# Kernel optimization log

Measured on AMD Instinct MI355X. Metric: run time of the kernel, lower is better.

Reference implementation:

```python
import jax, jax.numpy as jnp
import numpy as np

E = 65536      # num edges
T = 262144     # num triplets
H = 128        # hidden_channels
D = 64         # int_emb_size
C = 8          # basis_emb_size
NR = 6         # num_radial
NS = 7         # num_spherical
NB = 6         # len(bt_list) = num_BT + 1
BT_LIST = (-1, 0, 1, 2, 3, 4)
NBS = 1        # num_before_skip (also used for after-skip list in original code)


def setup_inputs() -> dict:
    key = jax.random.key(0)
    ks = iter(jax.random.split(key, 40))
    s = 0.05
    p = lambda shape: jax.random.normal(next(ks), shape, dtype=jnp.float32) * s
    inp = dict(
        x=jax.random.normal(next(ks), (E, H), dtype=jnp.float32),
        rbf=jax.random.normal(next(ks), (E, NR), dtype=jnp.float32),
        sbf=jax.random.normal(next(ks), (T, NS * NR), dtype=jnp.float32),
        idx_kj=jax.random.randint(next(ks), (T,), 0, E),
        idx_ji=jax.random.randint(next(ks), (T,), 0, E),
        bt=jax.random.randint(next(ks), (E,), 0, 5),
        lambda_d=1,
        alpha=jnp.float32(0.7),
        # per-branch stacked weights (6 branches)
        W_kj=p((NB, H, H)), b_kj=jnp.zeros((NB, H), jnp.float32),
        W_rbf1=p((NB, NR, C)), W_rbf2=p((NB, C, H)),
        W_sbf1=p((NB, NS * NR, C)), W_sbf2=p((NB, C, D)),
        W_down=p((NB, H, D)),
        W_ji=p((H, H)), b_ji=jnp.zeros((H,), jnp.float32),
        W_up=p((D, H)),
        rb1_w=p((NBS, H, H)), rb1_b=jnp.zeros((NBS, H), jnp.float32),
        rb2_w=p((NBS, H, H)), rb2_b=jnp.zeros((NBS, H), jnp.float32),
        W_lin=p((H, H)), b_lin=jnp.zeros((H,), jnp.float32),
        ra1_w=p((NBS, H, H)), ra1_b=jnp.zeros((NBS, H), jnp.float32),
        ra2_w=p((NBS, H, H)), ra2_b=jnp.zeros((NBS, H), jnp.float32),
    )
    return inp


def reference(x, rbf, sbf, idx_kj, idx_ji, bt, lambda_d, alpha,
              W_kj, b_kj, W_rbf1, W_rbf2, W_sbf1, W_sbf2, W_down,
              W_ji, b_ji, W_up, rb1_w, rb1_b, rb2_w, rb2_b,
              W_lin, b_lin, ra1_w, ra1_b, ra2_w, ra2_b):
    act = jax.nn.silu

    x_ji = act(x @ W_ji + b_ji)                                  # [E,H]

    # per-branch edge transforms, vectorized over the 6 branches (axis b)
    tmp = act(jnp.einsum('eh,bhg->beg', x, W_kj) + b_kj[:, None, :])   # [B,E,H]
    rbf_p = jnp.einsum('er,brc->bec', rbf, W_rbf1)                     # [B,E,C]
    rbf_p = jnp.einsum('bec,bcg->beg', rbf_p, W_rbf2)                  # [B,E,H]
    tmp = tmp * rbf_p
    down = act(jnp.einsum('beh,bhd->bed', tmp, W_down))                # [B,E,D]

    sbf_p = jnp.einsum('ts,bsc->btc', sbf, W_sbf1)                     # [B,T,C]
    sbf_p = jnp.einsum('btc,bcd->btd', sbf_p, W_sbf2)                  # [B,T,D]

    spe = down[:, idx_kj, :] * sbf_p                                   # [B,T,D]

    # last branch scattered with weight alpha
    x_kj_tot = alpha * jax.ops.segment_sum(spe[-1], idx_ji, num_segments=E)

    # per band-type masked scatter with weight (1 - alpha)
    bt_trip = bt[idx_kj]                                               # [T]
    for b, btv in enumerate(BT_LIST):
        m = (bt_trip == btv).astype(x.dtype)[:, None]
        x_kj_tot = x_kj_tot + (1.0 - alpha) * jax.ops.segment_sum(
            spe[b] * m, idx_ji, num_segments=E)

    x_kj = act(x_kj_tot @ W_up)                                        # [E,H]
    h = x_ji + x_kj
    for i in range(rb1_w.shape[0]):
        h = h + act(act(h @ rb1_w[i] + rb1_b[i]) @ rb2_w[i] + rb2_b[i])
    h = act(h @ W_lin + b_lin) + x
    for i in range(ra1_w.shape[0]):
        h = h + act(act(h @ ra1_w[i] + ra1_b[i]) @ ra2_w[i] + ra2_b[i])
    return h
```

## Files before the change

kernel.cpp:

```cpp
#include <hip/hip_runtime.h>
#include <hip/hip_bf16.h>
#include <stdint.h>

typedef __bf16 bf16_t;
typedef bf16_t bf16x8 __attribute__((ext_vector_type(8)));
typedef bf16_t bf16x2 __attribute__((ext_vector_type(2)));
typedef float f32x4 __attribute__((ext_vector_type(4)));

#define E_N 65536
#define T_N 262144

__device__ __forceinline__ float silu_f(float v) {
  return v / (1.0f + __expf(-v));
}

__device__ __forceinline__ int permrow(int n) {
  return (n & ~31) | ((n & 1) << 4) | ((n & 30) >> 1);
}

__device__ __forceinline__ uint32_t pack_bf16(float a, float b) {
  union { bf16x2 h; uint32_t u; } u;
  u.h[0] = (bf16_t)a; u.h[1] = (bf16_t)b;
  return u.u;
}

template<int KI, int NTJ>
__device__ __forceinline__ void gemm_tile(const bf16_t* A, const bf16_t* B,
                                          int mb, int nb, int l16, int q,
                                          f32x4 (&acc)[2][NTJ]) {
#pragma unroll
  for (int kt = 0; kt < KI; ++kt) {
    const int sw = ((kt * 4 + q) ^ l16) << 3;
    bf16x8 a0 = *(const bf16x8*)(A + ((mb + l16) << 7) + sw);
    bf16x8 a1 = *(const bf16x8*)(A + ((mb + 16 + l16) << 7) + sw);
#pragma unroll
    for (int tj = 0; tj < NTJ; ++tj) {
      bf16x8 b = *(const bf16x8*)(B + ((nb + tj * 16 + l16) << 7) + sw);
      acc[0][tj] = __builtin_amdgcn_mfma_f32_16x16x32_bf16(a0, b, acc[0][tj], 0, 0, 0);
      acc[1][tj] = __builtin_amdgcn_mfma_f32_16x16x32_bf16(a1, b, acc[1][tj], 0, 0, 0);
    }
  }
}

template<int ROWS, int K8>
__device__ __forceinline__ void load_wT(bf16_t* dst, const bf16_t* src, int tid) {
  const uint4* s = (const uint4*)src;
#pragma unroll
  for (int i = tid; i < ROWS * K8; i += 256) {
    const int n = i / K8, k8 = i % K8;
    const int row = permrow(n);
    *(uint4*)(dst + (row << 7) + ((k8 ^ (row & 15)) << 3)) = s[i];
  }
}

template<int C4>
__device__ __forceinline__ void stage_x(bf16_t* dst, const float* src, int tid) {
  const float4* g = (const float4*)src;
#pragma unroll
  for (int i = tid; i < 64 * C4; i += 256) {
    const int row = i / C4, c4 = i % C4;
    float4 v = g[i];
    bf16_t t[4] = {(bf16_t)v.x, (bf16_t)v.y, (bf16_t)v.z, (bf16_t)v.w};
    *(uint2*)(dst + (row << 7) + ((((c4 >> 1) ^ (row & 15)) << 3) | ((c4 & 1) << 2))) =
        *(const uint2*)t;
  }
}

__global__ void prep_kernel(
    const float* __restrict__ W_ji, const float* __restrict__ W_kj,
    const float* __restrict__ W_down, const float* __restrict__ W_up,
    const float* __restrict__ rb1, const float* __restrict__ rb2,
    const float* __restrict__ W_lin, const float* __restrict__ ra1,
    const float* __restrict__ ra2, const float* __restrict__ W_rbf1,
    const float* __restrict__ W_rbf2,
    bf16_t* __restrict__ wjiT, bf16_t* __restrict__ wkjT,
    bf16_t* __restrict__ wdownT, bf16_t* __restrict__ wupT,
    bf16_t* __restrict__ rb1T, bf16_t* __restrict__ rb2T,
    bf16_t* __restrict__ linT, bf16_t* __restrict__ ra1T,
    bf16_t* __restrict__ ra2T, bf16_t* __restrict__ wcb)
{
  const int tid = threadIdx.x;
  if (blockIdx.x >= 112) {
    const int o = (blockIdx.x - 112) * 256 + tid;
    if (o < 640) {
      const int b = o >> 7, n = o & 127;
      bf16_t t[8];
#pragma unroll
      for (int r = 0; r < 6; ++r) {
        const float* w1 = W_rbf1 + (b + 1) * 48 + r * 8;
        const float* w2 = W_rbf2 + (b + 1) * 1024 + n;
        float s = 0.f;
#pragma unroll
        for (int c = 0; c < 8; ++c) s += w1[c] * w2[c * 128];
        t[r] = (bf16_t)s;
      }
      t[6] = (bf16_t)0.f; t[7] = (bf16_t)0.f;
      *(uint4*)(wcb + (b * 128 + n) * 8) = *(const uint4*)t;
    }
    return;
  }
  const int c = blockIdx.x * 256 + tid;
  const float* src; bf16_t* dst; int n, k8, N, K;
  if (c < 22528) {
    const int m = c >> 11, w = c & 2047;
    n = w >> 4; k8 = w & 15; N = 128; K = 128;
    if (m == 0)      { src = W_ji;  dst = wjiT; }
    else if (m <= 5) { src = W_kj + m * 16384; dst = wkjT + (m - 1) * 16384; }
    else if (m == 6) { src = rb1;   dst = rb1T; }
    else if (m == 7) { src = rb2;   dst = rb2T; }
    else if (m == 8) { src = W_lin; dst = linT; }
    else if (m == 9) { src = ra1;   dst = ra1T; }
    else             { src = ra2;   dst = ra2T; }
  } else if (c < 27648) {
    const int m = (c - 22528) >> 10, w = (c - 22528) & 1023;
    n = w >> 4; k8 = w & 15; N = 64; K = 128;
    src = W_down + (m + 1) * 8192; dst = wdownT + m * 8192;
  } else {
    const int w = c - 27648;
    n = w >> 3; k8 = w & 7; N = 128; K = 64;
    src = W_up; dst = wupT;
  }
  bf16_t t[8];
#pragma unroll
  for (int j = 0; j < 8; ++j) t[j] = (bf16_t)src[(k8 * 8 + j) * N + n];
  *(uint4*)(dst + n * K + k8 * 8) = *(const uint4*)t;
}

__global__ __launch_bounds__(256, 2)
void edge_kernel(const float* __restrict__ x, const float* __restrict__ rbf,
                 const float* __restrict__ b_kj, const float* __restrict__ b_ji,
                 const bf16_t* __restrict__ wjiT, const bf16_t* __restrict__ wkjT,
                 const bf16_t* __restrict__ wdownT, const bf16_t* __restrict__ wcb,
                 bf16_t* __restrict__ x_ji_out, bf16_t* __restrict__ down)
{
  __shared__ bf16_t xA[64 * 128];
  __shared__ bf16_t Wb[128 * 128];
  __shared__ bf16_t tmpA[64 * 128];
  __shared__ bf16_t rbfA[64 * 40];
  __shared__ bf16_t WcB[128 * 40];
  __shared__ float biasS[128];

  const int tid = threadIdx.x;
  const int lane = tid & 63, wv = tid >> 6;
  const int q = lane >> 4, l16 = lane & 15;
  const int mb = (wv >> 1) * 32, nb = (wv & 1) * 64;
  const int R = blockIdx.x * 64;
  const int br = blockIdx.y;

  stage_x<32>(xA, x + (size_t)R * 128, tid);
  if (br == 0) {
    load_wT<128, 16>(Wb, wjiT, tid);
    if (tid < 128) biasS[tid] = b_ji[tid];
  } else {
    load_wT<128, 16>(Wb, wkjT + (br - 1) * 16384, tid);
    if (tid < 128) biasS[tid] = b_kj[br * 128 + tid];
    const uint4 z = {0, 0, 0, 0};
    if (tid < 64) {
      const float* rg = rbf + (size_t)(R + tid) * 6;
      bf16_t t[8] = {(bf16_t)rg[0], (bf16_t)rg[1], (bf16_t)rg[2],
                     (bf16_t)rg[3], (bf16_t)rg[4], (bf16_t)rg[5],
                     (bf16_t)0.f, (bf16_t)0.f};
      *(uint4*)(rbfA + tid * 40)      = *(const uint4*)t;
      *(uint4*)(rbfA + tid * 40 + 8)  = z;
      *(uint4*)(rbfA + tid * 40 + 16) = z;
      *(uint4*)(rbfA + tid * 40 + 24) = z;
    } else if (tid >= 128) {
      const int n = tid - 128;
      const int row = permrow(n);
      uint4 w = ((const uint4*)(wcb + (size_t)(br - 1) * 1024))[n];
      *(uint4*)(WcB + row * 40)      = w;
      *(uint4*)(WcB + row * 40 + 8)  = z;
      *(uint4*)(WcB + row * 40 + 16) = z;
      *(uint4*)(WcB + row * 40 + 24) = z;
    }
  }
  __syncthreads();

  f32x4 acc[2][4] = {};
  gemm_tile<4, 4>(xA, Wb, mb, nb, l16, q, acc);

  if (br == 0) {
#pragma unroll
    for (int ti = 0; ti < 2; ++ti)
#pragma unroll
      for (int r = 0; r < 4; ++r) {
        const int row = mb + ti * 16 + q * 4 + r;
#pragma unroll
        for (int gl = 0; gl < 2; ++gl) {
          const int col0 = nb + gl * 32 + 2 * l16;
          const float2 b2 = *(const float2*)&biasS[col0];
          *(uint32_t*)&x_ji_out[(size_t)(R + row) * 128 + col0] =
              pack_bf16(silu_f(acc[ti][2 * gl][r] + b2.x),
                        silu_f(acc[ti][2 * gl + 1][r] + b2.y));
        }
      }
    return;
  }

  f32x4 accr[2][4] = {};
  {
    bf16x8 a0 = *(const bf16x8*)(rbfA + (mb + l16) * 40 + q * 8);
    bf16x8 a1 = *(const bf16x8*)(rbfA + (mb + 16 + l16) * 40 + q * 8);
#pragma unroll
    for (int tj = 0; tj < 4; ++tj) {
      bf16x8 b = *(const bf16x8*)(WcB + (nb + tj * 16 + l16) * 40 + q * 8);
      accr[0][tj] = __builtin_amdgcn_mfma_f32_16x16x32_bf16(a0, b, accr[0][tj], 0, 0, 0);
      accr[1][tj] = __builtin_amdgcn_mfma_f32_16x16x32_bf16(a1, b, accr[1][tj], 0, 0, 0);
    }
  }

#pragma unroll
  for (int ti = 0; ti < 2; ++ti)
#pragma unroll
    for (int r = 0; r < 4; ++r) {
      const int row = mb + ti * 16 + q * 4 + r;
#pragma unroll
      for (int gl = 0; gl < 2; ++gl) {
        const int col0 = nb + gl * 32 + 2 * l16;
        const float2 b2 = *(const float2*)&biasS[col0];
        const float v0 = silu_f(acc[ti][2 * gl][r] + b2.x) * accr[ti][2 * gl][r];
        const float v1 = silu_f(acc[ti][2 * gl + 1][r] + b2.y) * accr[ti][2 * gl + 1][r];
        *(uint32_t*)&tmpA[(row << 7) + ((((col0 >> 3) ^ (row & 15)) << 3) | (col0 & 7))] =
            pack_bf16(v0, v1);
      }
    }
  __syncthreads();
  load_wT<64, 16>(xA, wdownT + (br - 1) * 8192, tid);
  __syncthreads();

  const int nb2 = (wv & 1) * 32;
  f32x4 acc2[2][2] = {};
  gemm_tile<4, 2>(tmpA, xA, mb, nb2, l16, q, acc2);
#pragma unroll
  for (int ti = 0; ti < 2; ++ti)
#pragma unroll
    for (int r = 0; r < 4; ++r) {
      const int row = mb + ti * 16 + q * 4 + r;
      const int col0 = nb2 + 2 * l16;
      *(uint32_t*)&down[((size_t)(br - 1) * E_N + R + row) * 64 + col0] =
          pack_bf16(silu_f(acc2[ti][0][r]), silu_f(acc2[ti][1][r]));
    }
}

__global__ __launch_bounds__(256, 4)
void triplet_kernel(const float* __restrict__ sbf, const int* __restrict__ idx_kj,
                    const int* __restrict__ idx_ji, const int* __restrict__ bt,
                    const float* __restrict__ alpha_p,
                    const float* __restrict__ Wsbf1, const float* __restrict__ Wsbf2,
                    const bf16_t* __restrict__ down, float* __restrict__ xkj)
{
  __shared__ float s_sbf[64 * 44];
  __shared__ float s_W1[2016];
  __shared__ float s_W2[3072];
  __shared__ float s_c8[64 * 16];
  __shared__ int s_kj[64], s_ji[64], s_bs[64];

  const int tid = threadIdx.x;
  const int base = blockIdx.x * 64;

  for (int i = tid; i < 2016; i += 256) s_W1[i] = Wsbf1[i];
  for (int i = tid; i < 3072; i += 256) s_W2[i] = Wsbf2[i];
  if (tid < 64) {
    const int kj = idx_kj[base + tid];
    s_kj[tid] = kj;
    s_ji[tid] = idx_ji[base + tid];
    s_bs[tid] = bt[kj] + 1;
  }
  {
    const float2* sg = (const float2*)(sbf + (size_t)base * 42);
    for (int i = tid; i < 64 * 21; i += 256) {
      const int r = i / 21, c2 = i - r * 21;
      const float2 v = sg[i];
      s_sbf[r * 44 + c2 * 2] = v.x;
      s_sbf[r * 44 + c2 * 2 + 1] = v.y;
    }
  }
  __syncthreads();

  {
    const int i = tid >> 2;
    const int brr = (tid >> 1) & 1;
    const int cg = tid & 1;
    const int b = brr ? s_bs[i] : 5;
    const float* w = &s_W1[b * 336 + cg * 4];
    const float* sb = &s_sbf[i * 44];
    float a0 = 0.f, a1 = 0.f, a2 = 0.f, a3 = 0.f;
#pragma unroll
    for (int s = 0; s < 42; ++s) {
      const float sv = sb[s];
      const float* ws = w + s * 8;
      a0 += sv * ws[0]; a1 += sv * ws[1]; a2 += sv * ws[2]; a3 += sv * ws[3];
    }
    float* dc = &s_c8[i * 16 + brr * 8 + cg * 4];
    dc[0] = a0; dc[1] = a1; dc[2] = a2; dc[3] = a3;
  }
  __syncthreads();

  const float alpha = alpha_p[0];
  const float oma = 1.f - alpha;
  const int wv = tid >> 6, j = tid & 63;
  float w5[8];
#pragma unroll
  for (int c = 0; c < 8; ++c) w5[c] = s_W2[5 * 512 + c * 64 + j];

#pragma unroll 4
  for (int ii = 0; ii < 16; ++ii) {
    const int i = wv * 16 + ii;
    const int b = s_bs[i];
    const int kj = s_kj[i];
    const int ji = s_ji[i];
    const float* c8 = &s_c8[i * 16];
    float d5 = 0.f, db = 0.f;
#pragma unroll
    for (int c = 0; c < 8; ++c) {
      d5 += c8[c] * w5[c];
      db += c8[8 + c] * s_W2[b * 512 + c * 64 + j];
    }
    const float g5 = (float)down[((size_t)4 * E_N + kj) * 64 + j];
    const float gb = (float)down[((size_t)(b - 1) * E_N + kj) * 64 + j];
    const float r = alpha * g5 * d5 + oma * gb * db;
    unsafeAtomicAdd(&xkj[(size_t)ji * 64 + j], r);
  }
}

__global__ __launch_bounds__(256, 2)
void epi_kernel(const float* __restrict__ x, const bf16_t* __restrict__ x_ji,
                const float* __restrict__ xkj,
                const bf16_t* __restrict__ wupT,
                const bf16_t* __restrict__ rb1T, const float* __restrict__ rb1_b,
                const bf16_t* __restrict__ rb2T, const float* __restrict__ rb2_b,
                const bf16_t* __restrict__ linT, const float* __restrict__ lin_b,
                const bf16_t* __restrict__ ra1T, const float* __restrict__ ra1_b,
                const bf16_t* __restrict__ ra2T, const float* __restrict__ ra2_b,
                float* __restrict__ out)
{
  __shared__ bf16_t bufA[64 * 128];
  __shared__ bf16_t bufB[64 * 128];
  __shared__ bf16_t Wb[128 * 128];
  __shared__ float biasS[128];

  const int tid = threadIdx.x;
  const int lane = tid & 63, wv = tid >> 6;
  const int q = lane >> 4, l16 = lane & 15;
  const int mb = (wv >> 1) * 32, nb = (wv & 1) * 64;
  const int R = blockIdx.x * 64;

  stage_x<16>(bufA, xkj + (size_t)R * 64, tid);
  load_wT<128, 8>(Wb, wupT, tid);
  __syncthreads();

  f32x4 hreg[2][4];
  {
    f32x4 acc[2][4] = {};
    gemm_tile<2, 4>(bufA, Wb, mb, nb, l16, q, acc);
#pragma unroll
    for (int ti = 0; ti < 2; ++ti)
#pragma unroll
      for (int r = 0; r < 4; ++r) {
        const int row = mb + ti * 16 + q * 4 + r;
#pragma unroll
        for (int gl = 0; gl < 2; ++gl) {
          const int col0 = nb + gl * 32 + 2 * l16;
          union { uint32_t u; bf16x2 h; } xj;
          xj.u = *(const uint32_t*)&x_ji[(size_t)(R + row) * 128 + col0];
          const float h0 = (float)xj.h[0] + silu_f(acc[ti][2 * gl][r]);
          const float h1 = (float)xj.h[1] + silu_f(acc[ti][2 * gl + 1][r]);
          hreg[ti][2 * gl][r] = h0;
          hreg[ti][2 * gl + 1][r] = h1;
          *(uint32_t*)&bufB[(row << 7) + ((((col0 >> 3) ^ (row & 15)) << 3) | (col0 & 7))] =
              pack_bf16(h0, h1);
        }
      }
  }

#define EPI_STAGE(ASRC, WSRC, BIAS, BODY)                                        \
  __syncthreads();                                                               \
  load_wT<128, 16>(Wb, WSRC, tid);                                               \
  if (tid < 128) biasS[tid] = BIAS[tid];                                         \
  __syncthreads();                                                               \
  {                                                                              \
    f32x4 acc[2][4] = {};                                                        \
    gemm_tile<4, 4>(ASRC, Wb, mb, nb, l16, q, acc);                              \
    _Pragma("unroll")                                                            \
    for (int ti = 0; ti < 2; ++ti)                                               \
      _Pragma("unroll")                                                          \
      for (int r = 0; r < 4; ++r) {                                              \
        const int row = mb + ti * 16 + q * 4 + r;                                \
        _Pragma("unroll")                                                        \
        for (int gl = 0; gl < 2; ++gl) {                                         \
          const int col0 = nb + gl * 32 + 2 * l16;                               \
          const float2 b2 = *(const float2*)&biasS[col0];                        \
          const float g0 = acc[ti][2 * gl][r] + b2.x;                            \
          const float g1 = acc[ti][2 * gl + 1][r] + b2.y;                        \
          BODY                                                                   \
        }                                                                        \
      }                                                                          \
  }

  EPI_STAGE(bufB, rb1T, rb1_b, {
    *(uint32_t*)&bufA[(row << 7) + ((((col0 >> 3) ^ (row & 15)) << 3) | (col0 & 7))] =
        pack_bf16(silu_f(g0), silu_f(g1));
  })

  EPI_STAGE(bufA, rb2T, rb2_b, {
    const float h0 = hreg[ti][2 * gl][r] + silu_f(g0);
    const float h1 = hreg[ti][2 * gl + 1][r] + silu_f(g1);
    hreg[ti][2 * gl][r] = h0; hreg[ti][2 * gl + 1][r] = h1;
    *(uint32_t*)&bufB[(row << 7) + ((((col0 >> 3) ^ (row & 15)) << 3) | (col0 & 7))] =
        pack_bf16(h0, h1);
  })

  EPI_STAGE(bufB, linT, lin_b, {
    const float2 xv = *(const float2*)&x[(size_t)(R + row) * 128 + col0];
    const float h0 = silu_f(g0) + xv.x;
    const float h1 = silu_f(g1) + xv.y;
    hreg[ti][2 * gl][r] = h0; hreg[ti][2 * gl + 1][r] = h1;
    *(uint32_t*)&bufA[(row << 7) + ((((col0 >> 3) ^ (row & 15)) << 3) | (col0 & 7))] =
        pack_bf16(h0, h1);
  })

  EPI_STAGE(bufA, ra1T, ra1_b, {
    *(uint32_t*)&bufB[(row << 7) + ((((col0 >> 3) ^ (row & 15)) << 3) | (col0 & 7))] =
        pack_bf16(silu_f(g0), silu_f(g1));
  })

  EPI_STAGE(bufB, ra2T, ra2_b, {
    float2 o;
    o.x = hreg[ti][2 * gl][r] + silu_f(g0);
    o.y = hreg[ti][2 * gl + 1][r] + silu_f(g1);
    *(float2*)&out[(size_t)(R + row) * 128 + col0] = o;
  })
#undef EPI_STAGE
}

extern "C" void kernel_launch(void* const* d_in, const int* in_sizes, int n_in,
                              void* d_out, int out_size, void* d_ws, size_t ws_size,
                              hipStream_t stream)
{
  (void)in_sizes; (void)n_in; (void)out_size; (void)ws_size;
  const float* x      = (const float*)d_in[0];
  const float* rbf    = (const float*)d_in[1];
  const float* sbf    = (const float*)d_in[2];
  const int*   idx_kj = (const int*)d_in[3];
  const int*   idx_ji = (const int*)d_in[4];
  const int*   bt     = (const int*)d_in[5];
  const float* alpha  = (const float*)d_in[7];
  const float* W_kj   = (const float*)d_in[8];
  const float* b_kj   = (const float*)d_in[9];
  const float* W_rbf1 = (const float*)d_in[10];
  const float* W_rbf2 = (const float*)d_in[11];
  const float* W_sbf1 = (const float*)d_in[12];
  const float* W_sbf2 = (const float*)d_in[13];
  const float* W_down = (const float*)d_in[14];
  const float* W_ji   = (const float*)d_in[15];
  const float* b_ji   = (const float*)d_in[16];
  const float* W_up   = (const float*)d_in[17];
  const float* rb1_w  = (const float*)d_in[18];
  const float* rb1_b  = (const float*)d_in[19];
  const float* rb2_w  = (const float*)d_in[20];
  const float* rb2_b  = (const float*)d_in[21];
  const float* W_lin  = (const float*)d_in[22];
  const float* b_lin  = (const float*)d_in[23];
  const float* ra1_w  = (const float*)d_in[24];
  const float* ra1_b  = (const float*)d_in[25];
  const float* ra2_w  = (const float*)d_in[26];
  const float* ra2_b  = (const float*)d_in[27];

  char* ws = (char*)d_ws;
  bf16_t* down   = (bf16_t*)(ws);
  bf16_t* x_ji   = (bf16_t*)(ws + 41943040);
  float*  xkj    = (float*) (ws + 58720256);
  char* wbase    = ws + 75497472;
  bf16_t* wjiT   = (bf16_t*)(wbase + 0);
  bf16_t* wkjT   = (bf16_t*)(wbase + 32768);
  bf16_t* wdownT = (bf16_t*)(wbase + 196608);
  bf16_t* wupT   = (bf16_t*)(wbase + 278528);
  bf16_t* rb1T   = (bf16_t*)(wbase + 294912);
  bf16_t* rb2T   = (bf16_t*)(wbase + 327680);
  bf16_t* linT   = (bf16_t*)(wbase + 360448);
  bf16_t* ra1T   = (bf16_t*)(wbase + 393216);
  bf16_t* ra2T   = (bf16_t*)(wbase + 425984);
  bf16_t* wcb    = (bf16_t*)(wbase + 458752);

  hipMemsetAsync(xkj, 0, (size_t)E_N * 64 * 4, stream);
  prep_kernel<<<115, 256, 0, stream>>>(W_ji, W_kj, W_down, W_up, rb1_w, rb2_w,
                                       W_lin, ra1_w, ra2_w, W_rbf1, W_rbf2,
                                       wjiT, wkjT, wdownT, wupT, rb1T, rb2T,
                                       linT, ra1T, ra2T, wcb);
  edge_kernel<<<dim3(E_N / 64, 6), 256, 0, stream>>>(x, rbf, b_kj, b_ji, wjiT,
                                                     wkjT, wdownT, wcb, x_ji, down);
  triplet_kernel<<<T_N / 64, 256, 0, stream>>>(sbf, idx_kj, idx_ji, bt, alpha,
                                               W_sbf1, W_sbf2, down, xkj);
  epi_kernel<<<E_N / 64, 256, 0, stream>>>(x, x_ji, xkj, wupT, rb1T, rb1_b,
                                           rb2T, rb2_b, linT, b_lin,
                                           ra1T, ra1_b, ra2T, ra2_b,
                                           (float*)d_out);
}
```

Baseline: 377.6 us.

## Fold sbf weights into MFMA GEMM and read weights directly from global

The two sbf projections are premultiplied per branch in the prep kernel, so the triplet kernel now runs them as a bf16 MFMA GEMM over all five branch outputs instead of scalar FP32 loops through an 8-wide intermediate. The edge and epilogue kernels stop staging weight matrices in shared memory and load MFMA B-operands straight from global or L2 in a permuted layout. This removes the shared weight copies and their barriers, and cuts shared memory use so launch bounds can allow more resident blocks. In exchange, weights are re-read from cache by every wave, and the sbf product is rounded to bf16, which adds precision error.

```diff
diff --git a/kernel.cpp b/kernel.cpp
--- a/kernel.cpp
+++ b/kernel.cpp
@@ -24,10 +24,11 @@
   return u.u;
 }
 
-template<int KI, int NTJ>
-__device__ __forceinline__ void gemm_tile(const bf16_t* A, const bf16_t* B,
-                                          int mb, int nb, int l16, int q,
-                                          f32x4 (&acc)[2][NTJ]) {
+template<int KI, int NTJ, int BS>
+__device__ __forceinline__ void gemm_bg(const bf16_t* A, const bf16_t* __restrict__ Bg,
+                                        int mb, int nb, int l16, int q,
+                                        f32x4 (&acc)[2][NTJ]) {
+  const bf16_t* bp = Bg + (nb + l16) * BS + q * 8;
 #pragma unroll
   for (int kt = 0; kt < KI; ++kt) {
     const int sw = ((kt * 4 + q) ^ l16) << 3;
@@ -35,21 +36,10 @@
     bf16x8 a1 = *(const bf16x8*)(A + ((mb + 16 + l16) << 7) + sw);
 #pragma unroll
     for (int tj = 0; tj < NTJ; ++tj) {
-      bf16x8 b = *(const bf16x8*)(B + ((nb + tj * 16 + l16) << 7) + sw);
+      bf16x8 b = *(const bf16x8*)(bp + tj * 16 * BS + kt * 32);
       acc[0][tj] = __builtin_amdgcn_mfma_f32_16x16x32_bf16(a0, b, acc[0][tj], 0, 0, 0);
       acc[1][tj] = __builtin_amdgcn_mfma_f32_16x16x32_bf16(a1, b, acc[1][tj], 0, 0, 0);
     }
-  }
-}
-
-template<int ROWS, int K8>
-__device__ __forceinline__ void load_wT(bf16_t* dst, const bf16_t* src, int tid) {
-  const uint4* s = (const uint4*)src;
-#pragma unroll
-  for (int i = tid; i < ROWS * K8; i += 256) {
-    const int n = i / K8, k8 = i % K8;
-    const int row = permrow(n);
-    *(uint4*)(dst + (row << 7) + ((k8 ^ (row & 15)) << 3)) = s[i];
   }
 }
 
@@ -72,61 +62,87 @@
     const float* __restrict__ rb1, const float* __restrict__ rb2,
     const float* __restrict__ W_lin, const float* __restrict__ ra1,
     const float* __restrict__ ra2, const float* __restrict__ W_rbf1,
-    const float* __restrict__ W_rbf2,
+    const float* __restrict__ W_rbf2, const float* __restrict__ W_sbf1,
+    const float* __restrict__ W_sbf2,
     bf16_t* __restrict__ wjiT, bf16_t* __restrict__ wkjT,
     bf16_t* __restrict__ wdownT, bf16_t* __restrict__ wupT,
     bf16_t* __restrict__ rb1T, bf16_t* __restrict__ rb2T,
     bf16_t* __restrict__ linT, bf16_t* __restrict__ ra1T,
-    bf16_t* __restrict__ ra2T, bf16_t* __restrict__ wcb)
+    bf16_t* __restrict__ ra2T, bf16_t* __restrict__ wcb,
+    bf16_t* __restrict__ wsT)
 {
   const int tid = threadIdx.x;
-  if (blockIdx.x >= 112) {
-    const int o = (blockIdx.x - 112) * 256 + tid;
+  const int bx = blockIdx.x;
+  if (bx < 112) {
+    const int c = bx * 256 + tid;
+    const float* src; bf16_t* dst; int n, k8, N, K;
+    if (c < 22528) {
+      const int m = c >> 11, w = c & 2047;
+      n = w >> 4; k8 = w & 15; N = 128; K = 128;
+      if (m == 0)      { src = W_ji;  dst = wjiT; }
+      else if (m <= 5) { src = W_kj + m * 16384; dst = wkjT + (m - 1) * 16384; }
+      else if (m == 6) { src = rb1;   dst = rb1T; }
+      else if (m == 7) { src = rb2;   dst = rb2T; }
+      else if (m == 8) { src = W_lin; dst = linT; }
+      else if (m == 9) { src = ra1;   dst = ra1T; }
+      else             { src = ra2;   dst = ra2T; }
+    } else if (c < 27648) {
+      const int m = (c - 22528) >> 10, w = (c - 22528) & 1023;
+      n = w >> 4; k8 = w & 15; N = 64; K = 128;
+      src = W_down + (m + 1) * 8192; dst = wdownT + m * 8192;
+    } else {
+      const int w = c - 27648;
+      n = w >> 3; k8 = w & 7; N = 128; K = 64;
+      src = W_up; dst = wupT;
+    }
+    bf16_t t[8];
+#pragma unroll
+    for (int j = 0; j < 8; ++j) t[j] = (bf16_t)src[(k8 * 8 + j) * N + n];
+    *(uint4*)(dst + permrow(n) * K + k8 * 8) = *(const uint4*)t;
+  } else if (bx < 115) {
+    const int o = (bx - 112) * 256 + tid;
     if (o < 640) {
-      const int b = o >> 7, n = o & 127;
-      bf16_t t[8];
+      const int slot = o >> 7, n = o & 127;
+      const int b = slot + 1;
+      bf16_t t[32];
+#pragma unroll
+      for (int k = 0; k < 32; ++k) t[k] = (bf16_t)0.f;
 #pragma unroll
       for (int r = 0; r < 6; ++r) {
-        const float* w1 = W_rbf1 + (b + 1) * 48 + r * 8;
-        const float* w2 = W_rbf2 + (b + 1) * 1024 + n;
         float s = 0.f;
 #pragma unroll
-        for (int c = 0; c < 8; ++c) s += w1[c] * w2[c * 128];
+        for (int c = 0; c < 8; ++c)
+          s += W_rbf1[b * 48 + r * 8 + c] * W_rbf2[b * 1024 + c * 128 + n];
         t[r] = (bf16_t)s;
       }
-      t[6] = (bf16_t)0.f; t[7] = (bf16_t)0.f;
-      *(uint4*)(wcb + (b * 128 + n) * 8) = *(const uint4*)t;
-    }
-    return;
-  }
-  const int c = blockIdx.x * 256 + tid;
-  const float* src; bf16_t* dst; int n, k8, N, K;
-  if (c < 22528) {
-    const int m = c >> 11, w = c & 2047;
-    n = w >> 4; k8 = w & 15; N = 128; K = 128;
-    if (m == 0)      { src = W_ji;  dst = wjiT; }
-    else if (m <= 5) { src = W_kj + m * 16384; dst = wkjT + (m - 1) * 16384; }
-    else if (m == 6) { src = rb1;   dst = rb1T; }
-    else if (m == 7) { src = rb2;   dst = rb2T; }
-    else if (m == 8) { src = W_lin; dst = linT; }
-    else if (m == 9) { src = ra1;   dst = ra1T; }
-    else             { src = ra2;   dst = ra2T; }
-  } else if (c < 27648) {
-    const int m = (c - 22528) >> 10, w = (c - 22528) & 1023;
-    n = w >> 4; k8 = w & 15; N = 64; K = 128;
-    src = W_down + (m + 1) * 8192; dst = wdownT + m * 8192;
+      bf16_t* dst = wcb + slot * 4096 + permrow(n) * 32;
+#pragma unroll
+      for (int g = 0; g < 4; ++g) *(uint4*)(dst + g * 8) = *(const uint4*)(t + g * 8);
+    }
   } else {
-    const int w = c - 27648;
-    n = w >> 3; k8 = w & 7; N = 128; K = 64;
-    src = W_up; dst = wupT;
-  }
-  bf16_t t[8];
-#pragma unroll
-  for (int j = 0; j < 8; ++j) t[j] = (bf16_t)src[(k8 * 8 + j) * N + n];
-  *(uint4*)(dst + n * K + k8 * 8) = *(const uint4*)t;
-}
-
-__global__ __launch_bounds__(256, 2)
+    const int o = (bx - 115) * 256 + tid;
+    if (o < 320) {
+      const int slot = o >> 6, j = o & 63;
+      const int b = slot + 1;
+      bf16_t t[64];
+#pragma unroll
+      for (int s = 0; s < 64; ++s) {
+        float v = 0.f;
+        if (s < 42) {
+#pragma unroll
+          for (int c = 0; c < 8; ++c)
+            v += W_sbf1[b * 336 + s * 8 + c] * W_sbf2[b * 512 + c * 64 + j];
+        }
+        t[s] = (bf16_t)v;
+      }
+      bf16_t* dst = wsT + (slot * 64 + permrow(j)) * 64;
+#pragma unroll
+      for (int g = 0; g < 8; ++g) *(uint4*)(dst + g * 8) = *(const uint4*)(t + g * 8);
+    }
+  }
+}
+
+__global__ __launch_bounds__(256, 4)
 void edge_kernel(const float* __restrict__ x, const float* __restrict__ rbf,
                  const float* __restrict__ b_kj, const float* __restrict__ b_ji,
                  const bf16_t* __restrict__ wjiT, const bf16_t* __restrict__ wkjT,
@@ -134,10 +150,8 @@
                  bf16_t* __restrict__ x_ji_out, bf16_t* __restrict__ down)
 {
   __shared__ bf16_t xA[64 * 128];
-  __shared__ bf16_t Wb[128 * 128];
   __shared__ bf16_t tmpA[64 * 128];
-  __shared__ bf16_t rbfA[64 * 40];
-  __shared__ bf16_t WcB[128 * 40];
+  __shared__ bf16_t rbfA[64 * 32];
   __shared__ float biasS[128];
 
   const int tid = threadIdx.x;
@@ -148,36 +162,23 @@
   const int br = blockIdx.y;
 
   stage_x<32>(xA, x + (size_t)R * 128, tid);
-  if (br == 0) {
-    load_wT<128, 16>(Wb, wjiT, tid);
-    if (tid < 128) biasS[tid] = b_ji[tid];
-  } else {
-    load_wT<128, 16>(Wb, wkjT + (br - 1) * 16384, tid);
-    if (tid < 128) biasS[tid] = b_kj[br * 128 + tid];
+  if (tid < 128) biasS[tid] = (br == 0) ? b_ji[tid] : b_kj[br * 128 + tid];
+  if (br != 0 && tid < 64) {
+    const float* rg = rbf + (size_t)(R + tid) * 6;
+    bf16_t t[8] = {(bf16_t)rg[0], (bf16_t)rg[1], (bf16_t)rg[2],
+                   (bf16_t)rg[3], (bf16_t)rg[4], (bf16_t)rg[5],
+                   (bf16_t)0.f, (bf16_t)0.f};
     const uint4 z = {0, 0, 0, 0};
-    if (tid < 64) {
-      const float* rg = rbf + (size_t)(R + tid) * 6;
-      bf16_t t[8] = {(bf16_t)rg[0], (bf16_t)rg[1], (bf16_t)rg[2],
-                     (bf16_t)rg[3], (bf16_t)rg[4], (bf16_t)rg[5],
-                     (bf16_t)0.f, (bf16_t)0.f};
-      *(uint4*)(rbfA + tid * 40)      = *(const uint4*)t;
-      *(uint4*)(rbfA + tid * 40 + 8)  = z;
-      *(uint4*)(rbfA + tid * 40 + 16) = z;
-      *(uint4*)(rbfA + tid * 40 + 24) = z;
-    } else if (tid >= 128) {
-      const int n = tid - 128;
-      const int row = permrow(n);
-      uint4 w = ((const uint4*)(wcb + (size_t)(br - 1) * 1024))[n];
-      *(uint4*)(WcB + row * 40)      = w;
-      *(uint4*)(WcB + row * 40 + 8)  = z;
-      *(uint4*)(WcB + row * 40 + 16) = z;
-      *(uint4*)(WcB + row * 40 + 24) = z;
-    }
+    bf16_t* dst = rbfA + tid * 32;
+#pragma unroll
+    for (int g = 0; g < 4; ++g) *(uint4*)(dst + g * 8) = z;
+    *(uint4*)(dst + ((tid & 3) << 3)) = *(const uint4*)t;
   }
   __syncthreads();
 
+  const bf16_t* WB = (br == 0) ? wjiT : wkjT + (size_t)(br - 1) * 16384;
   f32x4 acc[2][4] = {};
-  gemm_tile<4, 4>(xA, Wb, mb, nb, l16, q, acc);
+  gemm_bg<4, 4, 128>(xA, WB, mb, nb, l16, q, acc);
 
   if (br == 0) {
 #pragma unroll
@@ -199,11 +200,13 @@
 
   f32x4 accr[2][4] = {};
   {
-    bf16x8 a0 = *(const bf16x8*)(rbfA + (mb + l16) * 40 + q * 8);
-    bf16x8 a1 = *(const bf16x8*)(rbfA + (mb + 16 + l16) * 40 + q * 8);
+    const int sw = (q ^ (l16 & 3)) << 3;
+    bf16x8 a0 = *(const bf16x8*)(rbfA + ((mb + l16) << 5) + sw);
+    bf16x8 a1 = *(const bf16x8*)(rbfA + ((mb + 16 + l16) << 5) + sw);
+    const bf16_t* wb = wcb + (size_t)(br - 1) * 4096 + (nb + l16) * 32 + q * 8;
 #pragma unroll
     for (int tj = 0; tj < 4; ++tj) {
-      bf16x8 b = *(const bf16x8*)(WcB + (nb + tj * 16 + l16) * 40 + q * 8);
+      bf16x8 b = *(const bf16x8*)(wb + tj * 16 * 32);
       accr[0][tj] = __builtin_amdgcn_mfma_f32_16x16x32_bf16(a0, b, accr[0][tj], 0, 0, 0);
       accr[1][tj] = __builtin_amdgcn_mfma_f32_16x16x32_bf16(a1, b, accr[1][tj], 0, 0, 0);
     }
@@ -225,12 +228,10 @@
       }
     }
   __syncthreads();
-  load_wT<64, 16>(xA, wdownT + (br - 1) * 8192, tid);
-  __syncthreads();
 
   const int nb2 = (wv & 1) * 32;
   f32x4 acc2[2][2] = {};
-  gemm_tile<4, 2>(tmpA, xA, mb, nb2, l16, q, acc2);
+  gemm_bg<4, 2, 128>(tmpA, wdownT + (size_t)(br - 1) * 8192, mb, nb2, l16, q, acc2);
 #pragma unroll
   for (int ti = 0; ti < 2; ++ti)
 #pragma unroll
@@ -242,88 +243,90 @@
     }
 }
 
-__global__ __launch_bounds__(256, 4)
+__global__ __launch_bounds__(256, 3)
 void triplet_kernel(const float* __restrict__ sbf, const int* __restrict__ idx_kj,
                     const int* __restrict__ idx_ji, const int* __restrict__ bt,
-                    const float* __restrict__ alpha_p,
-                    const float* __restrict__ Wsbf1, const float* __restrict__ Wsbf2,
+                    const float* __restrict__ alpha_p, const bf16_t* __restrict__ wsT,
                     const bf16_t* __restrict__ down, float* __restrict__ xkj)
 {
-  __shared__ float s_sbf[64 * 44];
-  __shared__ float s_W1[2016];
-  __shared__ float s_W2[3072];
-  __shared__ float s_c8[64 * 16];
+  __shared__ bf16_t s_sbf[64 * 64];
+  __shared__ bf16_t spC[64 * 344];
   __shared__ int s_kj[64], s_ji[64], s_bs[64];
 
   const int tid = threadIdx.x;
+  const int lane = tid & 63, wv = tid >> 6;
+  const int q = lane >> 4, l16 = lane & 15;
   const int base = blockIdx.x * 64;
 
-  for (int i = tid; i < 2016; i += 256) s_W1[i] = Wsbf1[i];
-  for (int i = tid; i < 3072; i += 256) s_W2[i] = Wsbf2[i];
   if (tid < 64) {
     const int kj = idx_kj[base + tid];
     s_kj[tid] = kj;
     s_ji[tid] = idx_ji[base + tid];
-    s_bs[tid] = bt[kj] + 1;
-  }
-  {
-    const float2* sg = (const float2*)(sbf + (size_t)base * 42);
-    for (int i = tid; i < 64 * 21; i += 256) {
-      const int r = i / 21, c2 = i - r * 21;
-      const float2 v = sg[i];
-      s_sbf[r * 44 + c2 * 2] = v.x;
-      s_sbf[r * 44 + c2 * 2 + 1] = v.y;
-    }
+    s_bs[tid] = bt[kj];
+  }
+#pragma unroll
+  for (int it = 0; it < 2; ++it) {
+    const int i = tid + it * 256;
+    const int row = i >> 3, k8 = i & 7;
+    const float* sg = sbf + (size_t)(base + row) * 42 + k8 * 8;
+    bf16_t t[8];
+#pragma unroll
+    for (int jj = 0; jj < 8; ++jj)
+      t[jj] = (k8 * 8 + jj < 42) ? (bf16_t)sg[jj] : (bf16_t)0.f;
+    *(uint4*)(s_sbf + (row << 6) + ((k8 ^ (row & 7)) << 3)) = *(const uint4*)t;
   }
   __syncthreads();
 
-  {
-    const int i = tid >> 2;
-    const int brr = (tid >> 1) & 1;
-    const int cg = tid & 1;
-    const int b = brr ? s_bs[i] : 5;
-    const float* w = &s_W1[b * 336 + cg * 4];
-    const float* sb = &s_sbf[i * 44];
-    float a0 = 0.f, a1 = 0.f, a2 = 0.f, a3 = 0.f;
-#pragma unroll
-    for (int s = 0; s < 42; ++s) {
-      const float sv = sb[s];
-      const float* ws = w + s * 8;
-      a0 += sv * ws[0]; a1 += sv * ws[1]; a2 += sv * ws[2]; a3 += sv * ws[3];
-    }
-    float* dc = &s_c8[i * 16 + brr * 8 + cg * 4];
-    dc[0] = a0; dc[1] = a1; dc[2] = a2; dc[3] = a3;
-  }
+  const int mb = (wv & 1) * 32;
+  const int tb0 = (wv >> 1) * 10;
+  f32x4 acc[2][10] = {};
+#pragma unroll
+  for (int kt = 0; kt < 2; ++kt) {
+    const int sw = (((kt << 2) + q) ^ (l16 & 7)) << 3;
+    bf16x8 a0 = *(const bf16x8*)(s_sbf + ((mb + l16) << 6) + sw);
+    bf16x8 a1 = *(const bf16x8*)(s_sbf + ((mb + 16 + l16) << 6) + sw);
+    const bf16_t* bp = wsT + (tb0 * 16 + l16) * 64 + (kt << 5) + (q << 3);
+#pragma unroll
+    for (int tj = 0; tj < 10; ++tj) {
+      bf16x8 b = *(const bf16x8*)(bp + tj * 1024);
+      acc[0][tj] = __builtin_amdgcn_mfma_f32_16x16x32_bf16(a0, b, acc[0][tj], 0, 0, 0);
+      acc[1][tj] = __builtin_amdgcn_mfma_f32_16x16x32_bf16(a1, b, acc[1][tj], 0, 0, 0);
+    }
+  }
+#pragma unroll
+  for (int ti = 0; ti < 2; ++ti)
+#pragma unroll
+    for (int r = 0; r < 4; ++r) {
+      const int row = mb + ti * 16 + q * 4 + r;
+#pragma unroll
+      for (int tp = 0; tp < 5; ++tp) {
+        const int t0 = tb0 + 2 * tp;
+        const int col = (t0 >> 2) * 64 + (((t0 & 3) >> 1) << 5) + 2 * l16;
+        *(uint32_t*)&spC[row * 344 + col] =
+            pack_bf16(acc[ti][2 * tp][r], acc[ti][2 * tp + 1][r]);
+      }
+    }
   __syncthreads();
 
   const float alpha = alpha_p[0];
   const float oma = 1.f - alpha;
-  const int wv = tid >> 6, j = tid & 63;
-  float w5[8];
-#pragma unroll
-  for (int c = 0; c < 8; ++c) w5[c] = s_W2[5 * 512 + c * 64 + j];
-
+  const int j = lane;
 #pragma unroll 4
   for (int ii = 0; ii < 16; ++ii) {
-    const int i = wv * 16 + ii;
-    const int b = s_bs[i];
-    const int kj = s_kj[i];
-    const int ji = s_ji[i];
-    const float* c8 = &s_c8[i * 16];
-    float d5 = 0.f, db = 0.f;
-#pragma unroll
-    for (int c = 0; c < 8; ++c) {
-      d5 += c8[c] * w5[c];
-      db += c8[8 + c] * s_W2[b * 512 + c * 64 + j];
-    }
+    const int t = wv * 16 + ii;
+    const int slot = s_bs[t];
+    const int kj = s_kj[t];
+    const int ji = s_ji[t];
+    const float d5 = (float)spC[t * 344 + 256 + j];
+    const float db = (float)spC[t * 344 + slot * 64 + j];
     const float g5 = (float)down[((size_t)4 * E_N + kj) * 64 + j];
-    const float gb = (float)down[((size_t)(b - 1) * E_N + kj) * 64 + j];
+    const float gb = (float)down[((size_t)slot * E_N + kj) * 64 + j];
     const float r = alpha * g5 * d5 + oma * gb * db;
     unsafeAtomicAdd(&xkj[(size_t)ji * 64 + j], r);
   }
 }
 
-__global__ __launch_bounds__(256, 2)
+__global__ __launch_bounds__(256, 4)
 void epi_kernel(const float* __restrict__ x, const bf16_t* __restrict__ x_ji,
                 const float* __restrict__ xkj,
                 const bf16_t* __restrict__ wupT,
@@ -336,8 +339,7 @@
 {
   __shared__ bf16_t bufA[64 * 128];
   __shared__ bf16_t bufB[64 * 128];
-  __shared__ bf16_t Wb[128 * 128];
-  __shared__ float biasS[128];
+  __shared__ float biasAll[5 * 128];
 
   const int tid = threadIdx.x;
   const int lane = tid & 63, wv = tid >> 6;
@@ -346,13 +348,19 @@
   const int R = blockIdx.x * 64;
 
   stage_x<16>(bufA, xkj + (size_t)R * 64, tid);
-  load_wT<128, 8>(Wb, wupT, tid);
+  if (tid < 128) {
+    biasAll[tid]       = rb1_b[tid];
+    biasAll[128 + tid] = rb2_b[tid];
+    biasAll[256 + tid] = lin_b[tid];
+    biasAll[384 + tid] = ra1_b[tid];
+    biasAll[512 + tid] = ra2_b[tid];
+  }
   __syncthreads();
 
   f32x4 hreg[2][4];
   {
     f32x4 acc[2][4] = {};
-    gemm_tile<2, 4>(bufA, Wb, mb, nb, l16, q, acc);
+    gemm_bg<2, 4, 64>(bufA, wupT, mb, nb, l16, q, acc);
 #pragma unroll
     for (int ti = 0; ti < 2; ++ti)
 #pragma unroll
@@ -373,14 +381,11 @@
       }
   }
 
-#define EPI_STAGE(ASRC, WSRC, BIAS, BODY)                                        \
-  __syncthreads();                                                               \
-  load_wT<128, 16>(Wb, WSRC, tid);                                               \
-  if (tid < 128) biasS[tid] = BIAS[tid];                                         \
+#define EPI_STAGE(ASRC, WPTR, BROW, BODY)                                        \
   __syncthreads();                                                               \
   {                                                                              \
     f32x4 acc[2][4] = {};                                                        \
-    gemm_tile<4, 4>(ASRC, Wb, mb, nb, l16, q, acc);                              \
+    gemm_bg<4, 4, 128>(ASRC, WPTR, mb, nb, l16, q, acc);                         \
     _Pragma("unroll")                                                            \
     for (int ti = 0; ti < 2; ++ti)                                               \
       _Pragma("unroll")                                                          \
@@ -389,7 +394,7 @@
         _Pragma("unroll")                                                        \
         for (int gl = 0; gl < 2; ++gl) {                                         \
           const int col0 = nb + gl * 32 + 2 * l16;                               \
-          const float2 b2 = *(const float2*)&biasS[col0];                        \
+          const float2 b2 = *(const float2*)&biasAll[BROW * 128 + col0];         \
           const float g0 = acc[ti][2 * gl][r] + b2.x;                            \
           const float g1 = acc[ti][2 * gl + 1][r] + b2.y;                        \
           BODY                                                                   \
@@ -397,12 +402,12 @@
       }                                                                          \
   }
 
-  EPI_STAGE(bufB, rb1T, rb1_b, {
+  EPI_STAGE(bufB, rb1T, 0, {
     *(uint32_t*)&bufA[(row << 7) + ((((col0 >> 3) ^ (row & 15)) << 3) | (col0 & 7))] =
         pack_bf16(silu_f(g0), silu_f(g1));
   })
 
-  EPI_STAGE(bufA, rb2T, rb2_b, {
+  EPI_STAGE(bufA, rb2T, 1, {
     const float h0 = hreg[ti][2 * gl][r] + silu_f(g0);
     const float h1 = hreg[ti][2 * gl + 1][r] + silu_f(g1);
     hreg[ti][2 * gl][r] = h0; hreg[ti][2 * gl + 1][r] = h1;
@@ -410,7 +415,7 @@
         pack_bf16(h0, h1);
   })
 
-  EPI_STAGE(bufB, linT, lin_b, {
+  EPI_STAGE(bufB, linT, 2, {
     const float2 xv = *(const float2*)&x[(size_t)(R + row) * 128 + col0];
     const float h0 = silu_f(g0) + xv.x;
     const float h1 = silu_f(g1) + xv.y;
@@ -419,12 +424,12 @@
         pack_bf16(h0, h1);
   })
 
-  EPI_STAGE(bufA, ra1T, ra1_b, {
+  EPI_STAGE(bufA, ra1T, 3, {
     *(uint32_t*)&bufB[(row << 7) + ((((col0 >> 3) ^ (row & 15)) << 3) | (col0 & 7))] =
         pack_bf16(silu_f(g0), silu_f(g1));
   })
 
-  EPI_STAGE(bufB, ra2T, ra2_b, {
+  EPI_STAGE(bufB, ra2T, 4, {
     float2 o;
     o.x = hreg[ti][2 * gl][r] + silu_f(g0);
     o.y = hreg[ti][2 * gl + 1][r] + silu_f(g1);
@@ -481,16 +486,18 @@
   bf16_t* ra1T   = (bf16_t*)(wbase + 393216);
   bf16_t* ra2T   = (bf16_t*)(wbase + 425984);
   bf16_t* wcb    = (bf16_t*)(wbase + 458752);
+  bf16_t* wsT    = (bf16_t*)(wbase + 499712);
 
   hipMemsetAsync(xkj, 0, (size_t)E_N * 64 * 4, stream);
-  prep_kernel<<<115, 256, 0, stream>>>(W_ji, W_kj, W_down, W_up, rb1_w, rb2_w,
+  prep_kernel<<<117, 256, 0, stream>>>(W_ji, W_kj, W_down, W_up, rb1_w, rb2_w,
                                        W_lin, ra1_w, ra2_w, W_rbf1, W_rbf2,
+                                       W_sbf1, W_sbf2,
                                        wjiT, wkjT, wdownT, wupT, rb1T, rb2T,
-                                       linT, ra1T, ra2T, wcb);
+                                       linT, ra1T, ra2T, wcb, wsT);
   edge_kernel<<<dim3(E_N / 64, 6), 256, 0, stream>>>(x, rbf, b_kj, b_ji, wjiT,
                                                      wkjT, wdownT, wcb, x_ji, down);
   triplet_kernel<<<T_N / 64, 256, 0, stream>>>(sbf, idx_kj, idx_ji, bt, alpha,
-                                               W_sbf1, W_sbf2, down, xkj);
+                                               wsT, down, xkj);
   epi_kernel<<<E_N / 64, 256, 0, stream>>>(x, x_ji, xkj, wupT, rb1T, rb1_b,
                                            rb2T, rb2_b, linT, b_lin,
                                            ra1T, ra1_b, ra2T, ra2_b,
```

After: 444.2 us. 17.6% more time.
